# Kernel optimization log

Measured on AMD Instinct MI355X. Metric: run time of the kernel, lower is better.

The kernel has to match this reference:

```python
import jax, jax.numpy as jnp
import numpy as np

DIVISOR = 2.0
NEGATIVE_SLOPE = 0.01


def setup_inputs() -> dict:
    key = jax.random.key(0)
    k1, k2, k3 = jax.random.split(key, 3)
    x = jax.random.normal(k1, (32, 128, 130, 130), dtype=jnp.float32)
    weight = jax.random.normal(k2, (256, 128, 3, 3), dtype=jnp.float32) * 0.05
    bias = jax.random.normal(k3, (256,), dtype=jnp.float32)
    return {"x": x, "weight": weight, "bias": bias}


def reference(x, weight, bias):
    # conv2d, stride=1, padding=0 (VALID), NCHW / OIHW layout
    y = jax.lax.conv_general_dilated(
        x, weight,
        window_strides=(1, 1),
        padding='VALID',
        dimension_numbers=('NCHW', 'OIHW', 'NCHW'),
    )
    y = y + bias[None, :, None, None]
    y = y * (1.0 / DIVISOR)
    # fused LeakyReLU epilogue
    return jnp.where(y >= 0, y, y * NEGATIVE_SLOPE)
```

## Files before the change

### kernel.cpp

```cpp
#include <hip/hip_runtime.h>
#include <hip/hip_bf16.h>
#include <stdint.h>

typedef __bf16 bf16x8 __attribute__((ext_vector_type(8)));
typedef float  f32x4  __attribute__((ext_vector_type(4)));

#define NSLOPE 0.01f

#define NB   32
#define CIN  128
#define HIN  130
#define WIN  130
#define KOUT 256
#define POUT 128
#define QOUT 128
#define HWIN (HIN*WIN)

#define XP_BYTES 138444800ull
#define WP_ELEMS (2*3*3*KOUT*64)

#define WS_BYTES 32768
#define XS_BASE  65536
#define LDS_TOTAL 132096

__device__ __forceinline__ unsigned short f2bf(float f) {
    unsigned u = __builtin_bit_cast(unsigned, f);
    u += 0x7FFFu + ((u >> 16) & 1u);
    return (unsigned short)(u >> 16);
}

__device__ __forceinline__ void g2lds16(const void* g, void* l) {
    __builtin_amdgcn_global_load_lds(
        (const __attribute__((address_space(1))) void*)g,
        (__attribute__((address_space(3))) void*)l,
        16, 0, 0);
}

__global__ __launch_bounds__(256) void k_conv_x(const float* __restrict__ X,
                                                unsigned short* __restrict__ Xp) {
    __shared__ unsigned short tile[130*132];
    const int b = blockIdx.x;
    const int n = b / 130, h = b - n*130;
    const int tid = threadIdx.x;
    const size_t in_base = (size_t)n*(CIN*(size_t)HWIN) + (size_t)h*WIN;
    for (int fi = tid; fi < CIN*WIN; fi += 256) {
        int c = fi / WIN, w = fi - c*WIN;
        tile[w*132 + c] = f2bf(X[in_base + (size_t)c*HWIN + w]);
    }
    __syncthreads();
    unsigned short* outp = Xp + (size_t)b * (WIN*CIN);
    for (int oi = tid; oi < (WIN*CIN)/4; oi += 256) {
        int e = oi*4; int w = e >> 7; int c4 = e & 127;
        const unsigned short* t = &tile[w*132 + c4];
        ushort4 v; v.x = t[0]; v.y = t[1]; v.z = t[2]; v.w = t[3];
        *(ushort4*)(outp + e) = v;
    }
}

__global__ __launch_bounds__(256) void k_conv_w(const float* __restrict__ W,
                                                unsigned short* __restrict__ Wp) {
    int e = blockIdx.x*256 + threadIdx.x;
    if (e >= WP_ELEMS) return;
    int ci = e & 63;
    int k  = (e >> 6) & 255;
    int rsIdx = e >> 14;
    int cc = rsIdx / 9; int rem = rsIdx - cc*9; int r = rem / 3, s = rem - r*3;
    int c = cc*64 + ci;
    Wp[e] = f2bf(W[(size_t)k*1152 + (size_t)c*9 + r*3 + s]);
}

__device__ __forceinline__ void stage_w_half(const unsigned short* __restrict__ Wp,
                                             unsigned char* lds, int rsidx, int tid, int half) {
    const unsigned short* wbase = Wp + (size_t)rsidx * (KOUT*64);
    #pragma unroll
    for (int it = half*2; it < half*2 + 2; ++it) {
        const int t    = it*512 + tid;
        const int phys = t << 4;
        const int row  = phys >> 7;
        const int cib  = (phys & 127) ^ ((row & 7) << 4);
        g2lds16(wbase + (size_t)row*64 + (cib >> 1), lds + phys);
    }
}

__device__ __forceinline__ void stage_x4(const unsigned short* __restrict__ Xp,
                                         unsigned char* lds, int n, int p2, int cc, int tid) {
    #pragma unroll
    for (int it = 0; it < 9; ++it) {
        const int t = it*512 + tid;
        if (t < 4160) {
            const int phys = t << 4;
            const int g    = phys >> 7;
            const int rloc = g / 130;
            const int w    = g - 130*rloc;
            const int cib  = (phys & 127) ^ ((g & 7) << 4);
            const unsigned short* src =
                Xp + ((size_t)((n*HIN + p2 + rloc)*WIN + w))*CIN + cc*64 + (cib >> 1);
            g2lds16(src, lds + phys);
        }
    }
}

__global__ __launch_bounds__(512, 2) void k_conv_main(
    const unsigned short* __restrict__ Xp,
    const unsigned short* __restrict__ Wp,
    const float* __restrict__ bias,
    float* __restrict__ out)
{
    extern __shared__ __align__(16) unsigned char smem[];

    const int tid  = threadIdx.x;
    const int lane = tid & 63;
    const int wid  = tid >> 6;
    const int wm   = wid >> 2;
    const int wn   = wid & 3;
    const int l15  = lane & 15;
    const int kg   = lane >> 4;

    const int L     = ((blockIdx.x & 7) << 8) | (blockIdx.x >> 3);
    const int ppair = L & 63;
    const int n     = L >> 6;
    const int p2    = ppair << 1;

    unsigned char* xs = smem + XS_BASE;

    f32x4 acc[8][4];
    #pragma unroll
    for (int i = 0; i < 8; ++i)
        #pragma unroll
        for (int j = 0; j < 4; ++j)
            acc[i][j] = (f32x4){0.f, 0.f, 0.f, 0.f};

    stage_w_half(Wp, smem, 0, tid, 0);
    stage_w_half(Wp, smem, 0, tid, 1);
    stage_x4(Xp, xs, n, p2, 0, tid);
    asm volatile("s_waitcnt vmcnt(0)" ::: "memory");
    __builtin_amdgcn_s_barrier();

    for (int t = 0; t < 18; ++t) {
        const int cc  = t / 9;
        const int rem = t - cc*9;
        const int rr  = rem / 3;
        const int s   = rem - rr*3;
        unsigned char* wsR = smem + (t & 1)*WS_BYTES;
        const bool haveW   = (t + 1 < 18);
        unsigned char* wsW = smem + ((t + 1) & 1)*WS_BYTES;

        #pragma unroll
        for (int kq = 0; kq < 2; ++kq) {
            const int cib0 = kq*64 + kg*16;
            bf16x8 afA[4], afB[4], bx[4];

            #pragma unroll
            for (int mf = 0; mf < 4; ++mf) {
                const int row = wm*128 + mf*16 + l15;
                afA[mf] = *(const bf16x8*)(wsR + row*128 + (cib0 ^ ((row & 7) << 4)));
            }
            #pragma unroll
            for (int nf = 0; nf < 4; ++nf) {
                const int qq = wn*64 + nf*16 + l15;
                const int g  = ((qq >> 7) + rr)*130 + (qq & 127) + s;
                bx[nf] = *(const bf16x8*)(xs + g*128 + (cib0 ^ ((g & 7) << 4)));
            }
            if (haveW && kq == 0) stage_w_half(Wp, wsW, t + 1, tid, 0);
            __builtin_amdgcn_s_barrier();
            asm volatile("s_waitcnt lgkmcnt(0)" ::: "memory");
            __builtin_amdgcn_sched_barrier(0);
            __builtin_amdgcn_s_setprio(1);
            #pragma unroll
            for (int mf = 0; mf < 4; ++mf)
                #pragma unroll
                for (int nf = 0; nf < 4; ++nf)
                    acc[mf][nf] = __builtin_amdgcn_mfma_f32_16x16x32_bf16(
                        afA[mf], bx[nf], acc[mf][nf], 0, 0, 0);
            __builtin_amdgcn_s_setprio(0);
            __builtin_amdgcn_s_barrier();

            #pragma unroll
            for (int mf = 0; mf < 4; ++mf) {
                const int row = wm*128 + (mf + 4)*16 + l15;
                afB[mf] = *(const bf16x8*)(wsR + row*128 + (cib0 ^ ((row & 7) << 4)));
            }
            if (haveW && kq == 0) stage_w_half(Wp, wsW, t + 1, tid, 1);
            __builtin_amdgcn_s_barrier();
            asm volatile("s_waitcnt lgkmcnt(0)" ::: "memory");
            __builtin_amdgcn_sched_barrier(0);
            __builtin_amdgcn_s_setprio(1);
            #pragma unroll
            for (int mf = 0; mf < 4; ++mf)
                #pragma unroll
                for (int nf = 0; nf < 4; ++nf)
                    acc[mf + 4][nf] = __builtin_amdgcn_mfma_f32_16x16x32_bf16(
                        afB[mf], bx[nf], acc[mf + 4][nf], 0, 0, 0);
            __builtin_amdgcn_s_setprio(0);
            if (kq == 1)
                asm volatile("s_waitcnt vmcnt(0)" ::: "memory");
            __builtin_amdgcn_s_barrier();
        }

        if (t == 8) {
            stage_x4(Xp, xs, n, p2, 1, tid);
            asm volatile("s_waitcnt vmcnt(0)" ::: "memory");
            __builtin_amdgcn_s_barrier();
        }
    }

    #pragma unroll
    for (int mf = 0; mf < 8; ++mf) {
        const int kb = wm*128 + mf*16 + kg*4;
        const float4 bv = *(const float4*)(bias + kb);
        const float bj[4] = {bv.x, bv.y, bv.z, bv.w};
        #pragma unroll
        for (int nf = 0; nf < 4; ++nf) {
            const int qq = wn*64 + nf*16 + l15;
            const int pl = qq >> 7, q = qq & 127;
            const size_t base = (((size_t)n*KOUT + kb)*POUT + (p2 + pl))*QOUT + q;
            #pragma unroll
            for (int j = 0; j < 4; ++j) {
                float y = (acc[mf][nf][j] + bj[j]) * 0.5f;
                out[base + (size_t)j*(POUT*QOUT)] = (y >= 0.f) ? y : y*NSLOPE;
            }
        }
    }
}

extern "C" void kernel_launch(void* const* d_in, const int* in_sizes, int n_in,
                              void* d_out, int out_size, void* d_ws, size_t ws_size,
                              hipStream_t stream) {
    const float* X = (const float*)d_in[0];
    const float* W = (const float*)d_in[1];
    const float* B = (const float*)d_in[2];
    float* out = (float*)d_out;
    unsigned short* Xp = (unsigned short*)d_ws;
    unsigned short* Wp = (unsigned short*)((char*)d_ws + XP_BYTES);

    (void)hipFuncSetAttribute((const void*)k_conv_main,
                              hipFuncAttributeMaxDynamicSharedMemorySize, LDS_TOTAL);

    k_conv_x   <<<NB*HIN, 256, 0, stream>>>(X, Xp);
    k_conv_w   <<<(WP_ELEMS + 255)/256, 256, 0, stream>>>(W, Wp);
    k_conv_main<<<2048, 512, LDS_TOTAL, stream>>>(Xp, Wp, B, out);
}
```

Measured before the change: 444.5 us.

## Switch main conv GEMM to 32x32x16 MFMA with software-pipelined LDS loads

Replaces the 16x16x32 bf16 MFMA tiling with 32x32x16 MFMAs, giving each wave a 4x2 grid of 32x32 accumulator tiles. Per-row-tap iteration the A/B fragment loads are split into four k-slices and interleaved with the MFMA groups using partial lgkmcnt waits. The whole next weight slice is staged in one shot, and the intra-iteration barriers are reduced to a single one. The intent is fewer LDS reads per FLOP and better overlap of LDS latency with matrix math. In exchange there is more register pressure from holding all fragments, and the epilogue is remapped to the 32x32 output layout.

```diff
diff --git a/kernel.cpp b/kernel.cpp
--- a/kernel.cpp
+++ b/kernel.cpp
@@ -3,7 +3,7 @@
 #include <stdint.h>
 
 typedef __bf16 bf16x8 __attribute__((ext_vector_type(8)));
-typedef float  f32x4  __attribute__((ext_vector_type(4)));
+typedef float  f32x16 __attribute__((ext_vector_type(16)));
 
 #define NSLOPE 0.01f
 
@@ -15,6 +15,7 @@
 #define POUT 128
 #define QOUT 128
 #define HWIN (HIN*WIN)
+#define PQ   (POUT*QOUT)
 
 #define XP_BYTES 138444800ull
 #define WP_ELEMS (2*3*3*KOUT*64)
@@ -22,6 +23,9 @@
 #define WS_BYTES 32768
 #define XS_BASE  65536
 #define LDS_TOTAL 132096
+
+#define SB0()    __builtin_amdgcn_sched_barrier(0)
+#define LGKM(n)  asm volatile("s_waitcnt lgkmcnt(" #n ")" ::: "memory")
 
 __device__ __forceinline__ unsigned short f2bf(float f) {
     unsigned u = __builtin_bit_cast(unsigned, f);
@@ -69,11 +73,11 @@
     Wp[e] = f2bf(W[(size_t)k*1152 + (size_t)c*9 + r*3 + s]);
 }
 
-__device__ __forceinline__ void stage_w_half(const unsigned short* __restrict__ Wp,
-                                             unsigned char* lds, int rsidx, int tid, int half) {
+__device__ __forceinline__ void stage_w_all(const unsigned short* __restrict__ Wp,
+                                            unsigned char* lds, int rsidx, int tid) {
     const unsigned short* wbase = Wp + (size_t)rsidx * (KOUT*64);
     #pragma unroll
-    for (int it = half*2; it < half*2 + 2; ++it) {
+    for (int it = 0; it < 4; ++it) {
         const int t    = it*512 + tid;
         const int phys = t << 4;
         const int row  = phys >> 7;
@@ -113,8 +117,8 @@
     const int wid  = tid >> 6;
     const int wm   = wid >> 2;
     const int wn   = wid & 3;
-    const int l15  = lane & 15;
-    const int kg   = lane >> 4;
+    const int l31  = lane & 31;
+    const int hi16 = (lane >> 5) << 4;
 
     const int L     = ((blockIdx.x & 7) << 8) | (blockIdx.x >> 3);
     const int ppair = L & 63;
@@ -123,15 +127,21 @@
 
     unsigned char* xs = smem + XS_BASE;
 
-    f32x4 acc[8][4];
-    #pragma unroll
-    for (int i = 0; i < 8; ++i)
-        #pragma unroll
-        for (int j = 0; j < 4; ++j)
-            acc[i][j] = (f32x4){0.f, 0.f, 0.f, 0.f};
-
-    stage_w_half(Wp, smem, 0, tid, 0);
-    stage_w_half(Wp, smem, 0, tid, 1);
+    const int rowA0 = wm*128 + l31;
+    const int swA   = (l31 & 7) << 4;
+    int aOff[4];
+    #pragma unroll
+    for (int k16 = 0; k16 < 4; ++k16)
+        aOff[k16] = rowA0*128 + ((k16*32 + hi16) ^ swA);
+
+    f32x16 acc[4][2];
+    #pragma unroll
+    for (int i = 0; i < 4; ++i)
+        #pragma unroll
+        for (int j = 0; j < 2; ++j)
+            acc[i][j] = (f32x16)(0.f);
+
+    stage_w_all(Wp, smem, 0, tid);
     stage_x4(Xp, xs, n, p2, 0, tid);
     asm volatile("s_waitcnt vmcnt(0)" ::: "memory");
     __builtin_amdgcn_s_barrier();
@@ -142,60 +152,87 @@
         const int rr  = rem / 3;
         const int s   = rem - rr*3;
         unsigned char* wsR = smem + (t & 1)*WS_BYTES;
+        unsigned char* wsW = smem + ((t + 1) & 1)*WS_BYTES;
         const bool haveW   = (t + 1 < 18);
-        unsigned char* wsW = smem + ((t + 1) & 1)*WS_BYTES;
-
-        #pragma unroll
-        for (int kq = 0; kq < 2; ++kq) {
-            const int cib0 = kq*64 + kg*16;
-            bf16x8 afA[4], afB[4], bx[4];
-
-            #pragma unroll
-            for (int mf = 0; mf < 4; ++mf) {
-                const int row = wm*128 + mf*16 + l15;
-                afA[mf] = *(const bf16x8*)(wsR + row*128 + (cib0 ^ ((row & 7) << 4)));
-            }
-            #pragma unroll
-            for (int nf = 0; nf < 4; ++nf) {
-                const int qq = wn*64 + nf*16 + l15;
-                const int g  = ((qq >> 7) + rr)*130 + (qq & 127) + s;
-                bx[nf] = *(const bf16x8*)(xs + g*128 + (cib0 ^ ((g & 7) << 4)));
-            }
-            if (haveW && kq == 0) stage_w_half(Wp, wsW, t + 1, tid, 0);
-            __builtin_amdgcn_s_barrier();
-            asm volatile("s_waitcnt lgkmcnt(0)" ::: "memory");
-            __builtin_amdgcn_sched_barrier(0);
-            __builtin_amdgcn_s_setprio(1);
-            #pragma unroll
-            for (int mf = 0; mf < 4; ++mf)
-                #pragma unroll
-                for (int nf = 0; nf < 4; ++nf)
-                    acc[mf][nf] = __builtin_amdgcn_mfma_f32_16x16x32_bf16(
-                        afA[mf], bx[nf], acc[mf][nf], 0, 0, 0);
-            __builtin_amdgcn_s_setprio(0);
-            __builtin_amdgcn_s_barrier();
-
-            #pragma unroll
-            for (int mf = 0; mf < 4; ++mf) {
-                const int row = wm*128 + (mf + 4)*16 + l15;
-                afB[mf] = *(const bf16x8*)(wsR + row*128 + (cib0 ^ ((row & 7) << 4)));
-            }
-            if (haveW && kq == 0) stage_w_half(Wp, wsW, t + 1, tid, 1);
-            __builtin_amdgcn_s_barrier();
-            asm volatile("s_waitcnt lgkmcnt(0)" ::: "memory");
-            __builtin_amdgcn_sched_barrier(0);
-            __builtin_amdgcn_s_setprio(1);
-            #pragma unroll
-            for (int mf = 0; mf < 4; ++mf)
-                #pragma unroll
-                for (int nf = 0; nf < 4; ++nf)
-                    acc[mf + 4][nf] = __builtin_amdgcn_mfma_f32_16x16x32_bf16(
-                        afB[mf], bx[nf], acc[mf + 4][nf], 0, 0, 0);
-            __builtin_amdgcn_s_setprio(0);
-            if (kq == 1)
-                asm volatile("s_waitcnt vmcnt(0)" ::: "memory");
-            __builtin_amdgcn_s_barrier();
-        }
+
+        const int g0  = ((wn >> 1) + rr)*130 + (wn & 1)*64 + l31 + s;
+        const int swB = (g0 & 7) << 4;
+        int bOff[4];
+        #pragma unroll
+        for (int k16 = 0; k16 < 4; ++k16)
+            bOff[k16] = g0*128 + ((k16*32 + hi16) ^ swB);
+
+        bf16x8 A0[4], A1[4], A2[4], A3[4], B0[2], B1[2], B2[2], B3[2];
+
+        #pragma unroll
+        for (int mf = 0; mf < 4; ++mf) A0[mf] = *(const bf16x8*)(wsR + aOff[0] + mf*4096);
+        #pragma unroll
+        for (int nf = 0; nf < 2; ++nf) B0[nf] = *(const bf16x8*)(xs + bOff[0] + nf*4096);
+        SB0();
+        #pragma unroll
+        for (int mf = 0; mf < 4; ++mf) A1[mf] = *(const bf16x8*)(wsR + aOff[1] + mf*4096);
+        #pragma unroll
+        for (int nf = 0; nf < 2; ++nf) B1[nf] = *(const bf16x8*)(xs + bOff[1] + nf*4096);
+        if (haveW) stage_w_all(Wp, wsW, t + 1, tid);
+        SB0();
+
+        LGKM(6); SB0();
+        __builtin_amdgcn_s_setprio(1);
+        #pragma unroll
+        for (int mf = 0; mf < 4; ++mf)
+            #pragma unroll
+            for (int nf = 0; nf < 2; ++nf)
+                acc[mf][nf] = __builtin_amdgcn_mfma_f32_32x32x16_bf16(
+                    A0[mf], B0[nf], acc[mf][nf], 0, 0, 0);
+        __builtin_amdgcn_s_setprio(0);
+        SB0();
+
+        #pragma unroll
+        for (int mf = 0; mf < 4; ++mf) A2[mf] = *(const bf16x8*)(wsR + aOff[2] + mf*4096);
+        #pragma unroll
+        for (int nf = 0; nf < 2; ++nf) B2[nf] = *(const bf16x8*)(xs + bOff[2] + nf*4096);
+        SB0();
+        #pragma unroll
+        for (int mf = 0; mf < 4; ++mf) A3[mf] = *(const bf16x8*)(wsR + aOff[3] + mf*4096);
+        #pragma unroll
+        for (int nf = 0; nf < 2; ++nf) B3[nf] = *(const bf16x8*)(xs + bOff[3] + nf*4096);
+        SB0();
+
+        LGKM(12); SB0();
+        __builtin_amdgcn_s_setprio(1);
+        #pragma unroll
+        for (int mf = 0; mf < 4; ++mf)
+            #pragma unroll
+            for (int nf = 0; nf < 2; ++nf)
+                acc[mf][nf] = __builtin_amdgcn_mfma_f32_32x32x16_bf16(
+                    A1[mf], B1[nf], acc[mf][nf], 0, 0, 0);
+        __builtin_amdgcn_s_setprio(0);
+        SB0();
+
+        LGKM(6); SB0();
+        __builtin_amdgcn_s_setprio(1);
+        #pragma unroll
+        for (int mf = 0; mf < 4; ++mf)
+            #pragma unroll
+            for (int nf = 0; nf < 2; ++nf)
+                acc[mf][nf] = __builtin_amdgcn_mfma_f32_32x32x16_bf16(
+                    A2[mf], B2[nf], acc[mf][nf], 0, 0, 0);
+        __builtin_amdgcn_s_setprio(0);
+        SB0();
+
+        LGKM(0); SB0();
+        __builtin_amdgcn_s_setprio(1);
+        #pragma unroll
+        for (int mf = 0; mf < 4; ++mf)
+            #pragma unroll
+            for (int nf = 0; nf < 2; ++nf)
+                acc[mf][nf] = __builtin_amdgcn_mfma_f32_32x32x16_bf16(
+                    A3[mf], B3[nf], acc[mf][nf], 0, 0, 0);
+        __builtin_amdgcn_s_setprio(0);
+        SB0();
+
+        asm volatile("s_waitcnt vmcnt(0)" ::: "memory");
+        __builtin_amdgcn_s_barrier();
 
         if (t == 8) {
             stage_x4(Xp, xs, n, p2, 1, tid);
@@ -204,20 +241,25 @@
         }
     }
 
-    #pragma unroll
-    for (int mf = 0; mf < 8; ++mf) {
-        const int kb = wm*128 + mf*16 + kg*4;
-        const float4 bv = *(const float4*)(bias + kb);
-        const float bj[4] = {bv.x, bv.y, bv.z, bv.w};
-        #pragma unroll
-        for (int nf = 0; nf < 4; ++nf) {
-            const int qq = wn*64 + nf*16 + l15;
-            const int pl = qq >> 7, q = qq & 127;
-            const size_t base = (((size_t)n*KOUT + kb)*POUT + (p2 + pl))*QOUT + q;
-            #pragma unroll
-            for (int j = 0; j < 4; ++j) {
-                float y = (acc[mf][nf][j] + bj[j]) * 0.5f;
-                out[base + (size_t)j*(POUT*QOUT)] = (y >= 0.f) ? y : y*NSLOPE;
+    const int hi = lane >> 5;
+    #pragma unroll
+    for (int mf = 0; mf < 4; ++mf) {
+        const int kb0 = wm*128 + mf*32;
+        #pragma unroll
+        for (int rq = 0; rq < 4; ++rq) {
+            const int kr = kb0 + rq*8 + hi*4;
+            const float4 bv = *(const float4*)(bias + kr);
+            const float bj[4] = {bv.x, bv.y, bv.z, bv.w};
+            #pragma unroll
+            for (int nf = 0; nf < 2; ++nf) {
+                const int qcol = (wn & 1)*64 + nf*32 + l31;
+                const int pl   = wn >> 1;
+                const size_t base = (((size_t)n*KOUT + kr)*POUT + (p2 + pl))*QOUT + qcol;
+                #pragma unroll
+                for (int j = 0; j < 4; ++j) {
+                    float y = (acc[mf][nf][rq*4 + j] + bj[j]) * 0.5f;
+                    out[base + (size_t)j*PQ] = (y >= 0.f) ? y : y*NSLOPE;
+                }
             }
         }
     }
```

After: 451.3 us. Within noise of the previous version (+1.5%).
